# Optimization experiments

Hardware: AMD Instinct MI355X
Metric: run time of the kernel (lower is better)

The kernel has to match this reference:

```python
import jax, jax.numpy as jnp
import numpy as np
from jax import lax

N, T, D_IN = 8192, 64, 64
R = 256            # reservoir_dim
K = 3              # diffusion hops
D_OUT = 64
E = 131072
LEAK = 0.3
SPECTRAL_RADIUS = 0.9
SPARSITY = 0.9


def setup_inputs() -> dict:
    key = jax.random.key(0)
    kx, ke = jax.random.split(key)
    rng = np.random.default_rng(0)

    # ESN fixed buffers (match torch init: randn*0.1; sparse randn scaled to rho)
    W_in = (rng.standard_normal((R, D_IN)) * 0.1).astype(np.float32)
    W_res = rng.standard_normal((R, R)).astype(np.float32)
    mask = rng.random((R, R)) < SPARSITY
    W_res[mask] = 0.0
    rho = float(np.abs(np.linalg.eigvals(W_res)).max())
    if rho > 1e-8:
        W_res = W_res * (SPECTRAL_RADIUS / rho)

    # readout: Linear((K+1)*R -> 2*D_OUT), GELU, Linear(2*D_OUT -> D_OUT), LayerNorm
    fan1 = (K + 1) * R
    W1 = (rng.standard_normal((2 * D_OUT, fan1)) / np.sqrt(fan1)).astype(np.float32)
    b1 = np.zeros((2 * D_OUT,), np.float32)
    W2 = (rng.standard_normal((D_OUT, 2 * D_OUT)) / np.sqrt(2 * D_OUT)).astype(np.float32)
    b2 = np.zeros((D_OUT,), np.float32)
    gamma = np.ones((D_OUT,), np.float32)
    beta = np.zeros((D_OUT,), np.float32)

    x = jax.random.normal(kx, (N, T, D_IN), dtype=jnp.float32)
    edge_index = jax.random.randint(ke, (2, E), 0, N, dtype=jnp.int64)

    return {
        "x": x,
        "edge_index": edge_index,
        "W_in": jnp.asarray(W_in),
        "W_res": jnp.asarray(W_res),
        "W1": jnp.asarray(W1), "b1": jnp.asarray(b1),
        "W2": jnp.asarray(W2), "b2": jnp.asarray(b2),
        "gamma": jnp.asarray(gamma), "beta": jnp.asarray(beta),
    }


def _esn(x, W_in, W_res):
    # x: [N, T, D_IN] -> final reservoir state [N, R]
    x_proj = jnp.einsum("ntd,rd->tnr", x, W_in)  # [T, N, R]

    def step(h, xp_t):
        h_new = jnp.tanh(xp_t + h @ W_res.T)
        return (1.0 - LEAK) * h + LEAK * h_new, None

    h0 = jnp.zeros((x.shape[0], W_res.shape[0]), dtype=x.dtype)
    h, _ = lax.scan(step, h0, x_proj)
    return h


def _norm_adj(edge_index, n_nodes):
    # symmetric D^{-1/2} A D^{-1/2}; dedup handled by idempotent .set
    row = jnp.concatenate([edge_index[0], edge_index[1]])
    col = jnp.concatenate([edge_index[1], edge_index[0]])
    A_bin = jnp.zeros((n_nodes, n_nodes), jnp.float32).at[row, col].set(1.0)
    deg = A_bin.sum(axis=1)
    dinv = jnp.where(deg > 0, 1.0 / jnp.sqrt(jnp.maximum(deg, 1e-12)), 0.0)
    dinv = jnp.minimum(dinv, 1e6)
    return dinv[:, None] * A_bin * dinv[None, :]


def reference(x, edge_index, W_in, W_res, W1, b1, W2, b2, gamma, beta):
    h = _esn(x, W_in, W_res)                    # [N, R]
    A = _norm_adj(edge_index, x.shape[0])       # [N, N]

    diffused = [h]
    h_k = h
    for _ in range(K):
        h_k = A @ h_k
        diffused.append(h_k)
    cat = jnp.concatenate(diffused, axis=-1)    # [N, (K+1)*R]

    z = jax.nn.gelu(cat @ W1.T + b1, approximate=False)
    z = z @ W2.T + b2                           # [N, D_OUT]
    mu = z.mean(axis=-1, keepdims=True)
    var = z.var(axis=-1, keepdims=True)
    z = (z - mu) / jnp.sqrt(var + 1e-5)
    return z * gamma + beta
```

## Files before the change

kernel.cpp:

```cpp
#include <hip/hip_runtime.h>
#include <hip/hip_bf16.h>
#include <hip/hip_fp16.h>
#include <math.h>

#define NN    8192
#define TT    64
#define DIN   64
#define RR    256
#define DOUT  64
#define HID   128
#define CATD  1024
#define NE    131072
#define MASKW 256
#define MAXD  256
#define HROW  328

typedef __attribute__((ext_vector_type(8))) short    s16x8;
typedef __attribute__((ext_vector_type(8))) _Float16 f16x8;
typedef __attribute__((ext_vector_type(4))) float    f32x4;

static __device__ __forceinline__ unsigned short f2bs(float f) {
  union { __hip_bfloat16 b; unsigned short u; } cv;
  cv.b = __float2bfloat16(f);
  return cv.u;
}
static __device__ __forceinline__ unsigned int pack2bf(float a, float b) {
  return (unsigned int)f2bs(a) | ((unsigned int)f2bs(b) << 16);
}
static __device__ __forceinline__ unsigned int pack2h(float a, float b) {
  return (unsigned int)__half_as_ushort(__float2half(a))
       | ((unsigned int)__half_as_ushort(__float2half(b)) << 16);
}


__global__ __launch_bounds__(256) void zero_mask_kernel(uint4* mask4, int n4) {
  int i = blockIdx.x * 256 + threadIdx.x;
  if (i < n4) mask4[i] = make_uint4(0u, 0u, 0u, 0u);
}

__global__ __launch_bounds__(256) void edge_kernel(const int* __restrict__ eidx,
                                                   unsigned int* __restrict__ mask) {
  int e = blockIdx.x * 256 + threadIdx.x;
  if (e < NE) {
    int u = eidx[e];
    int v = eidx[NE + e];
    atomicOr(&mask[(size_t)u * MASKW + (v >> 5)], 1u << (v & 31));
    atomicOr(&mask[(size_t)v * MASKW + (u >> 5)], 1u << (u & 31));
  }
}

__global__ __launch_bounds__(256) void nbrlist_kernel(const unsigned int* __restrict__ mask,
                                                      unsigned short* __restrict__ nbrlist,
                                                      int* __restrict__ nbrcnt,
                                                      float* __restrict__ dinv) {
  __shared__ int wsum[4];
  const int n = blockIdx.x;
  const int tid = threadIdx.x;
  const int lane = tid & 63;
  const int w = tid >> 6;
  unsigned int m = mask[(size_t)n * MASKW + tid];
  const int c = __popc(m);
  int inc = c;
#pragma unroll
  for (int d = 1; d < 64; d <<= 1) {
    int v = __shfl_up(inc, d, 64);
    if (lane >= d) inc += v;
  }
  if (lane == 63) wsum[w] = inc;
  __syncthreads();
  int base = 0;
  for (int i = 0; i < w; ++i) base += wsum[i];
  int off = base + inc - c;
  while (m) {
    int b = __ffs(m) - 1;
    m &= m - 1;
    if (off < MAXD) nbrlist[(size_t)n * MAXD + off] = (unsigned short)(tid * 32 + b);
    ++off;
  }
  if (tid == 255) {
    int tot = base + inc;
    nbrcnt[n] = tot < MAXD ? tot : MAXD;
    dinv[n] = (tot > 0) ? fminf(rsqrtf((float)tot), 1e6f) : 0.0f;
  }
}

__global__ __launch_bounds__(256) void cvt_weights_kernel(
    const float* __restrict__ Wres, const float* __restrict__ Win,
    const float* __restrict__ W1, const float* __restrict__ W2,
    unsigned short* __restrict__ wresh, unsigned short* __restrict__ winh,
    unsigned short* __restrict__ W1h, unsigned short* __restrict__ W2h) {
  int i = blockIdx.x * 256 + threadIdx.x;
  if (i < 65536) wresh[i] = f2bs(Wres[i]);
  else if (i < 81920) winh[i - 65536] = f2bs(Win[i - 65536]);
  else if (i < 212992) W1h[i - 81920] = __half_as_ushort(__float2half(W1[i - 81920]));
  else if (i < 221184) W2h[i - 212992] = __half_as_ushort(__float2half(W2[i - 212992]));
}

__global__ __launch_bounds__(512, 4) void esn_mfma_kernel(
    const float* __restrict__ x,
    const unsigned short* __restrict__ winh,
    const unsigned short* __restrict__ wresh,
    unsigned short* __restrict__ cat)
{
  __shared__ unsigned short hs[2][16][HROW];
  const int tid  = threadIdx.x;
  const int lane = tid & 63;
  const int w    = tid >> 6;
  const int lr   = lane & 15;
  const int lg   = lane >> 4;
  const int sn   = tid >> 5;
  const int sq   = tid & 31;
  const long gn0 = (long)blockIdx.x * 16;
  const int bx   = (lr >> 3) & 1;
  const int lgx  = lg ^ bx;
  const int lgw  = (lg >> 1) ^ bx;
  const int bs   = (sn >> 3) & 1;

  s16x8 waug[2][10];
#pragma unroll
  for (int rt = 0; rt < 2; ++rt) {
    const int r = w * 32 + rt * 16 + lr;
#pragma unroll
    for (int kt = 0; kt < 8; ++kt)
      waug[rt][kt] = *(const s16x8*)(wresh + r * RR + kt * 32 + lg * 8);
#pragma unroll
    for (int kt = 8; kt < 10; ++kt)
      waug[rt][kt] = *(const s16x8*)(winh + r * DIN + (kt - 8) * 32 + lg * 8);
  }

  unsigned short* const rd0 = &hs[0][0][0] + lr * HROW + lgx * 8;
  unsigned short* const rd1 = &hs[1][0][0] + lr * HROW + lgx * 8;
  unsigned short* const wh0 = &hs[0][0][0] + lr * HROW + (w * 4 + lgw) * 8 + (lg & 1) * 4;
  unsigned short* const wh1 = &hs[1][0][0] + lr * HROW + (w * 4 + lgw) * 8 + (lg & 1) * 4;
  unsigned short* const xs0 = &hs[0][0][0] + sn * HROW + (32 + ((sq >> 2) ^ bs)) * 8 + (sq & 3) * 2;
  unsigned short* const xs1 = &hs[1][0][0] + sn * HROW + (32 + ((sq >> 2) ^ bs)) * 8 + (sq & 3) * 2;

  for (int i = tid; i < 16 * HROW / 2; i += 512) ((unsigned int*)hs[0])[i] = 0u;

  const float* xrow = x + (gn0 + sn) * (long)(TT * DIN) + sq * 2;
  float2 xr0 = *(const float2*)(xrow);
  float2 xr1 = *(const float2*)(xrow + DIN);
  __syncthreads();
  *(unsigned int*)xs0 = pack2bf(xr0.x, xr0.y);
  xr0 = *(const float2*)(xrow + 2 * DIN);

  f32x4 hreg[2];
  hreg[0] = (f32x4){0.f, 0.f, 0.f, 0.f};
  hreg[1] = (f32x4){0.f, 0.f, 0.f, 0.f};
  __syncthreads();

#define ESN_STEP(RD, WH, XS, XRS, XRL, TNEXT)                                        \
  {                                                                                  \
    f32x4 a0e = (f32x4){0.f,0.f,0.f,0.f}, a0o = a0e, a1e = a0e, a1o = a0e;           \
    __builtin_amdgcn_s_setprio(1);                                                   \
    _Pragma("unroll")                                                                \
    for (int kt = 0; kt < 10; kt += 2) {                                             \
      const s16x8 hbe = *(const s16x8*)(RD + kt * 32);                               \
      const s16x8 hbo = *(const s16x8*)(RD + (kt + 1) * 32);                         \
      a0e = __builtin_amdgcn_mfma_f32_16x16x32_bf16(waug[0][kt], hbe, a0e, 0, 0, 0); \
      a1e = __builtin_amdgcn_mfma_f32_16x16x32_bf16(waug[1][kt], hbe, a1e, 0, 0, 0); \
      a0o = __builtin_amdgcn_mfma_f32_16x16x32_bf16(waug[0][kt+1], hbo, a0o, 0, 0, 0);\
      a1o = __builtin_amdgcn_mfma_f32_16x16x32_bf16(waug[1][kt+1], hbo, a1o, 0, 0, 0);\
    }                                                                                \
    __builtin_amdgcn_s_setprio(0);                                                   \
    *(unsigned int*)(XS) = pack2bf(XRS.x, XRS.y);                 \
    XRL = *(const float2*)(xrow + (TNEXT) * DIN);                      \
    _Pragma("unroll")                                                                \
    for (int rt = 0; rt < 2; ++rt) {                                                 \
      const f32x4 ae = rt ? a1e : a0e;                                               \
      const f32x4 ao = rt ? a1o : a0o;                                               \
      f32x4 hn;                                                                      \
      _Pragma("unroll")                                                              \
      for (int i = 0; i < 4; ++i) {                                                  \
        const float sacc = ae[i] + ao[i];                                            \
        const float e = __builtin_amdgcn_exp2f(sacc * 2.8853900817779268f);          \
        const float rc = __builtin_amdgcn_rcpf(e + 1.0f);                            \
        hn[i] = fmaf(-0.6f, rc, fmaf(0.7f, hreg[rt][i], 0.3f));                      \
      }                                                                              \
      hreg[rt] = hn;                                                                 \
      *(uint2*)(WH + rt * 16) =                                                      \
          make_uint2(pack2bf(hn[0], hn[1]), pack2bf(hn[2], hn[3]));                  \
    }                                                                                \
  }

  for (int tc = 0; tc < TT / 2; ++tc) {
    const int t = tc * 2;
    const int tla = (t + 3 < TT) ? t + 3 : TT - 1;
    ESN_STEP(rd0, wh1, xs1, xr1, xr1, tla);
    __syncthreads();
    const int tlb = (t + 4 < TT) ? t + 4 : TT - 1;
    ESN_STEP(rd1, wh0, xs0, xr0, xr0, tlb);
    __syncthreads();
  }
#undef ESN_STEP

#pragma unroll
  for (int rt = 0; rt < 2; ++rt) {
    *(uint2*)(cat + (gn0 + lr) * CATD + w * 32 + rt * 16 + lg * 4) =
        make_uint2(pack2h(hreg[rt][0], hreg[rt][1]), pack2h(hreg[rt][2], hreg[rt][3]));
  }
}

__global__ __launch_bounds__(256) void spmv_kernel(
    const unsigned short* __restrict__ nbrlist, const int* __restrict__ nbrcnt,
    const float* __restrict__ dinv, unsigned short* __restrict__ cat, int hop)
{
  const int wv   = threadIdx.x >> 6;
  const int lane = threadIdx.x & 63;
  const int half = lane >> 5;
  const int li   = lane & 31;
  const int n    = blockIdx.x * 8 + wv * 2 + half;
  const int cnt  = nbrcnt[n];
  const __half* in = (const __half*)cat + (size_t)(hop - 1) * RR;
  float acc[8];
#pragma unroll
  for (int k = 0; k < 8; ++k) acc[k] = 0.0f;

  for (int c0 = 0; c0 < cnt; c0 += 32) {
    const int m = (cnt - c0 < 32) ? cnt - c0 : 32;
    int idx = 0; float dv = 0.f;
    if (li < m) {
      idx = (int)nbrlist[(size_t)n * MAXD + c0 + li];
      dv  = dinv[idx];
    }
#pragma unroll 8
    for (int i = 0; i < m; ++i) {
      const int   j  = __shfl(idx, half * 32 + i, 64);
      const float wj = __shfl(dv,  half * 32 + i, 64);
      const uint4 u  = *(const uint4*)(in + (size_t)j * CATD + li * 8);
      const float2 f0 = __half22float2(*(const __half2*)&u.x);
      const float2 f1 = __half22float2(*(const __half2*)&u.y);
      const float2 f2 = __half22float2(*(const __half2*)&u.z);
      const float2 f3 = __half22float2(*(const __half2*)&u.w);
      acc[0] += wj * f0.x; acc[1] += wj * f0.y;
      acc[2] += wj * f1.x; acc[3] += wj * f1.y;
      acc[4] += wj * f2.x; acc[5] += wj * f2.y;
      acc[6] += wj * f3.x; acc[7] += wj * f3.y;
    }
  }
  const float dn = dinv[n];
  uint4 o;
  o.x = pack2h(acc[0] * dn, acc[1] * dn);
  o.y = pack2h(acc[2] * dn, acc[3] * dn);
  o.z = pack2h(acc[4] * dn, acc[5] * dn);
  o.w = pack2h(acc[6] * dn, acc[7] * dn);
  *(uint4*)(cat + (size_t)n * CATD + (size_t)hop * RR + li * 8) = o;
}

__global__ __launch_bounds__(256) void readout_kernel(
    const unsigned short* __restrict__ cat,
    const unsigned short* __restrict__ W1h,
    const float* __restrict__ b1,
    const unsigned short* __restrict__ W2h,
    const float* __restrict__ b2, const float* __restrict__ gamma,
    const float* __restrict__ beta, float* __restrict__ out)
{
  __shared__ unsigned short z1[32][136];
  __shared__ float z2[32][68];
  const int tid  = threadIdx.x;
  const int lane = tid & 63;
  const int w    = tid >> 6;
  const int lr   = lane & 15;
  const int lg   = lane >> 4;
  const long gn0 = (long)blockIdx.x * 32;

  f32x4 a00 = (f32x4){0.f,0.f,0.f,0.f}, a01 = a00, a10 = a00, a11 = a00;
  const unsigned short* arow0 = cat + (gn0 + lr) * CATD;
  const unsigned short* arow1 = cat + (gn0 + 16 + lr) * CATD;
  const unsigned short* brow0 = W1h + (w * 32 + lr) * CATD;
  const unsigned short* brow1 = W1h + (w * 32 + 16 + lr) * CATD;
#pragma unroll 8
  for (int kt = 0; kt < 32; ++kt) {
    const f16x8 af0 = *(const f16x8*)(arow0 + kt * 32 + lg * 8);
    const f16x8 af1 = *(const f16x8*)(arow1 + kt * 32 + lg * 8);
    const f16x8 bf0 = *(const f16x8*)(brow0 + kt * 32 + lg * 8);
    const f16x8 bf1 = *(const f16x8*)(brow1 + kt * 32 + lg * 8);
    a00 = __builtin_amdgcn_mfma_f32_16x16x32_f16(af0, bf0, a00, 0, 0, 0);
    a01 = __builtin_amdgcn_mfma_f32_16x16x32_f16(af0, bf1, a01, 0, 0, 0);
    a10 = __builtin_amdgcn_mfma_f32_16x16x32_f16(af1, bf0, a10, 0, 0, 0);
    a11 = __builtin_amdgcn_mfma_f32_16x16x32_f16(af1, bf1, a11, 0, 0, 0);
  }
  const float is2 = 0.70710678118654752f;
#pragma unroll
  for (int nt = 0; nt < 2; ++nt) {
#pragma unroll
    for (int ht = 0; ht < 2; ++ht) {
      const int hid = w * 32 + ht * 16 + lr;
      const float bb = b1[hid];
      const f32x4 a = nt ? (ht ? a11 : a10) : (ht ? a01 : a00);
#pragma unroll
      for (int i = 0; i < 4; ++i) {
        const float v = a[i] + bb;
        const float g = 0.5f * v * (1.0f + erff(v * is2));
        z1[nt * 16 + lg * 4 + i][hid] = __half_as_ushort(__float2half(g));
      }
    }
  }
  __syncthreads();

  f32x4 c20 = (f32x4){0.f,0.f,0.f,0.f}, c21 = c20;
  const unsigned short* w2row = W2h + (w * 16 + lr) * HID;
#pragma unroll
  for (int kt = 0; kt < 4; ++kt) {
    const f16x8 bf  = *(const f16x8*)(w2row + kt * 32 + lg * 8);
    const f16x8 af0 = *(const f16x8*)(&z1[lr][kt * 32 + lg * 8]);
    const f16x8 af1 = *(const f16x8*)(&z1[16 + lr][kt * 32 + lg * 8]);
    c20 = __builtin_amdgcn_mfma_f32_16x16x32_f16(af0, bf, c20, 0, 0, 0);
    c21 = __builtin_amdgcn_mfma_f32_16x16x32_f16(af1, bf, c21, 0, 0, 0);
  }
  {
    const float bb = b2[w * 16 + lr];
#pragma unroll
    for (int i = 0; i < 4; ++i) {
      z2[lg * 4 + i][w * 16 + lr]      = c20[i] + bb;
      z2[16 + lg * 4 + i][w * 16 + lr] = c21[i] + bb;
    }
  }
  __syncthreads();

  {
    const int n = tid >> 3;
    const int c = tid & 7;
    float v[8], s = 0.0f, s2 = 0.0f;
#pragma unroll
    for (int k2 = 0; k2 < 8; ++k2) {
      v[k2] = z2[n][c + 8 * k2];
      s += v[k2]; s2 += v[k2] * v[k2];
    }
#pragma unroll
    for (int m = 1; m < 8; m <<= 1) {
      s  += __shfl_xor(s,  m, 64);
      s2 += __shfl_xor(s2, m, 64);
    }
    const float mu  = s * (1.0f / 64.0f);
    const float var = s2 * (1.0f / 64.0f) - mu * mu;
    const float inv = rsqrtf(var + 1e-5f);
    float* orow = out + (gn0 + n) * DOUT;
#pragma unroll
    for (int k2 = 0; k2 < 8; ++k2)
      orow[c + 8 * k2] = (v[k2] - mu) * inv * gamma[c + 8 * k2] + beta[c + 8 * k2];
  }
}


extern "C" void kernel_launch(void* const* d_in, const int* in_sizes, int n_in,
                              void* d_out, int out_size, void* d_ws, size_t ws_size,
                              hipStream_t stream) {
  const float* x     = (const float*)d_in[0];
  const int*   eidx  = (const int*)d_in[1];
  const float* W_in  = (const float*)d_in[2];
  const float* W_res = (const float*)d_in[3];
  const float* W1    = (const float*)d_in[4];
  const float* b1    = (const float*)d_in[5];
  const float* W2    = (const float*)d_in[6];
  const float* b2    = (const float*)d_in[7];
  const float* gamma = (const float*)d_in[8];
  const float* beta  = (const float*)d_in[9];
  float* out = (float*)d_out;

  char* ws = (char*)d_ws;
  size_t off = 0;
  auto alloc = [&](size_t bytes) {
    void* p = ws + off;
    off += (bytes + 255) & ~(size_t)255;
    return p;
  };
  unsigned int*   mask    = (unsigned int*)  alloc((size_t)NN * MASKW * 4);
  unsigned short* cat     = (unsigned short*)alloc((size_t)NN * CATD * 2);
  unsigned short* nbrlist = (unsigned short*)alloc((size_t)NN * MAXD * 2);
  int*            nbrcnt  = (int*)           alloc((size_t)NN * 4);
  float*          dinv    = (float*)         alloc((size_t)NN * 4);
  unsigned short* wresh   = (unsigned short*)alloc((size_t)RR * RR * 2);
  unsigned short* winh    = (unsigned short*)alloc((size_t)RR * DIN * 2);
  unsigned short* W1h     = (unsigned short*)alloc((size_t)HID * CATD * 2);
  unsigned short* W2h     = (unsigned short*)alloc((size_t)DOUT * HID * 2);

  zero_mask_kernel<<<2048, 256, 0, stream>>>((uint4*)mask, NN * MASKW / 4);
  edge_kernel<<<NE / 256, 256, 0, stream>>>(eidx, mask);
  nbrlist_kernel<<<NN, 256, 0, stream>>>(mask, nbrlist, nbrcnt, dinv);
  cvt_weights_kernel<<<864, 256, 0, stream>>>(W_res, W_in, W1, W2, wresh, winh, W1h, W2h);

  esn_mfma_kernel<<<NN / 16, 512, 0, stream>>>(x, winh, wresh, cat);

  for (int k = 1; k <= 3; ++k)
    spmv_kernel<<<NN / 8, 256, 0, stream>>>(nbrlist, nbrcnt, dinv, cat, k);

  readout_kernel<<<NN / 32, 256, 0, stream>>>(cat, W1h, b1, W2h, b2, gamma, beta, out);
}
```

Before: 193.0 us.

## Gather SpMV neighbor features from an FP8 shadow copy and fuse setup kernels

```diff
diff --git a/kernel.cpp b/kernel.cpp
--- a/kernel.cpp
+++ b/kernel.cpp
@@ -14,10 +14,12 @@
 #define MASKW 256
 #define MAXD  256
 #define HROW  328
+#define C8ROW 768
 
 typedef __attribute__((ext_vector_type(8))) short    s16x8;
 typedef __attribute__((ext_vector_type(8))) _Float16 f16x8;
 typedef __attribute__((ext_vector_type(4))) float    f32x4;
+typedef __attribute__((ext_vector_type(2))) float    f32x2;
 
 static __device__ __forceinline__ unsigned short f2bs(float f) {
   union { __hip_bfloat16 b; unsigned short u; } cv;
@@ -31,11 +33,26 @@
   return (unsigned int)__half_as_ushort(__float2half(a))
        | ((unsigned int)__half_as_ushort(__float2half(b)) << 16);
 }
-
-
-__global__ __launch_bounds__(256) void zero_mask_kernel(uint4* mask4, int n4) {
+static __device__ __forceinline__ unsigned int pack4fp8(float a, float b, float c, float d) {
+  unsigned int p = 0;
+  p = __builtin_amdgcn_cvt_pk_fp8_f32(a, b, (int)p, false);
+  p = __builtin_amdgcn_cvt_pk_fp8_f32(c, d, (int)p, true);
+  return p;
+}
+
+
+__global__ __launch_bounds__(256) void setup_kernel(
+    uint4* __restrict__ mask4,
+    const float* __restrict__ Wres, const float* __restrict__ Win,
+    const float* __restrict__ W1, const float* __restrict__ W2,
+    unsigned short* __restrict__ wresh, unsigned short* __restrict__ winh,
+    unsigned short* __restrict__ W1h, unsigned short* __restrict__ W2h) {
   int i = blockIdx.x * 256 + threadIdx.x;
-  if (i < n4) mask4[i] = make_uint4(0u, 0u, 0u, 0u);
+  mask4[i] = make_uint4(0u, 0u, 0u, 0u);
+  if (i < 65536) wresh[i] = f2bs(Wres[i]);
+  else if (i < 81920) winh[i - 65536] = f2bs(Win[i - 65536]);
+  else if (i < 212992) W1h[i - 81920] = __half_as_ushort(__float2half(W1[i - 81920]));
+  else if (i < 221184) W2h[i - 212992] = __half_as_ushort(__float2half(W2[i - 212992]));
 }
 
 __global__ __launch_bounds__(256) void edge_kernel(const int* __restrict__ eidx,
@@ -84,23 +101,12 @@
   }
 }
 
-__global__ __launch_bounds__(256) void cvt_weights_kernel(
-    const float* __restrict__ Wres, const float* __restrict__ Win,
-    const float* __restrict__ W1, const float* __restrict__ W2,
-    unsigned short* __restrict__ wresh, unsigned short* __restrict__ winh,
-    unsigned short* __restrict__ W1h, unsigned short* __restrict__ W2h) {
-  int i = blockIdx.x * 256 + threadIdx.x;
-  if (i < 65536) wresh[i] = f2bs(Wres[i]);
-  else if (i < 81920) winh[i - 65536] = f2bs(Win[i - 65536]);
-  else if (i < 212992) W1h[i - 81920] = __half_as_ushort(__float2half(W1[i - 81920]));
-  else if (i < 221184) W2h[i - 212992] = __half_as_ushort(__float2half(W2[i - 212992]));
-}
-
 __global__ __launch_bounds__(512, 4) void esn_mfma_kernel(
     const float* __restrict__ x,
     const unsigned short* __restrict__ winh,
     const unsigned short* __restrict__ wresh,
-    unsigned short* __restrict__ cat)
+    unsigned short* __restrict__ cat,
+    unsigned char* __restrict__ cat8)
 {
   __shared__ unsigned short hs[2][16][HROW];
   const int tid  = threadIdx.x;
@@ -198,12 +204,15 @@
   for (int rt = 0; rt < 2; ++rt) {
     *(uint2*)(cat + (gn0 + lr) * CATD + w * 32 + rt * 16 + lg * 4) =
         make_uint2(pack2h(hreg[rt][0], hreg[rt][1]), pack2h(hreg[rt][2], hreg[rt][3]));
+    *(unsigned int*)(cat8 + (gn0 + lr) * C8ROW + w * 32 + rt * 16 + lg * 4) =
+        pack4fp8(hreg[rt][0], hreg[rt][1], hreg[rt][2], hreg[rt][3]);
   }
 }
 
 __global__ __launch_bounds__(256) void spmv_kernel(
     const unsigned short* __restrict__ nbrlist, const int* __restrict__ nbrcnt,
-    const float* __restrict__ dinv, unsigned short* __restrict__ cat, int hop)
+    const float* __restrict__ dinv, unsigned short* __restrict__ cat,
+    unsigned char* __restrict__ cat8, int hop)
 {
   const int wv   = threadIdx.x >> 6;
   const int lane = threadIdx.x & 63;
@@ -211,7 +220,7 @@
   const int li   = lane & 31;
   const int n    = blockIdx.x * 8 + wv * 2 + half;
   const int cnt  = nbrcnt[n];
-  const __half* in = (const __half*)cat + (size_t)(hop - 1) * RR;
+  const unsigned char* in8 = cat8 + (size_t)(hop - 1) * RR;
   float acc[8];
 #pragma unroll
   for (int k = 0; k < 8; ++k) acc[k] = 0.0f;
@@ -227,24 +236,32 @@
     for (int i = 0; i < m; ++i) {
       const int   j  = __shfl(idx, half * 32 + i, 64);
       const float wj = __shfl(dv,  half * 32 + i, 64);
-      const uint4 u  = *(const uint4*)(in + (size_t)j * CATD + li * 8);
-      const float2 f0 = __half22float2(*(const __half2*)&u.x);
-      const float2 f1 = __half22float2(*(const __half2*)&u.y);
-      const float2 f2 = __half22float2(*(const __half2*)&u.z);
-      const float2 f3 = __half22float2(*(const __half2*)&u.w);
-      acc[0] += wj * f0.x; acc[1] += wj * f0.y;
-      acc[2] += wj * f1.x; acc[3] += wj * f1.y;
-      acc[4] += wj * f2.x; acc[5] += wj * f2.y;
-      acc[6] += wj * f3.x; acc[7] += wj * f3.y;
+      const uint2 u  = *(const uint2*)(in8 + (size_t)j * C8ROW + li * 8);
+      const f32x2 f0 = __builtin_amdgcn_cvt_pk_f32_fp8((int)u.x, false);
+      const f32x2 f1 = __builtin_amdgcn_cvt_pk_f32_fp8((int)u.x, true);
+      const f32x2 f2 = __builtin_amdgcn_cvt_pk_f32_fp8((int)u.y, false);
+      const f32x2 f3 = __builtin_amdgcn_cvt_pk_f32_fp8((int)u.y, true);
+      acc[0] += wj * f0[0]; acc[1] += wj * f0[1];
+      acc[2] += wj * f1[0]; acc[3] += wj * f1[1];
+      acc[4] += wj * f2[0]; acc[5] += wj * f2[1];
+      acc[6] += wj * f3[0]; acc[7] += wj * f3[1];
     }
   }
   const float dn = dinv[n];
+#pragma unroll
+  for (int k = 0; k < 8; ++k) acc[k] *= dn;
   uint4 o;
-  o.x = pack2h(acc[0] * dn, acc[1] * dn);
-  o.y = pack2h(acc[2] * dn, acc[3] * dn);
-  o.z = pack2h(acc[4] * dn, acc[5] * dn);
-  o.w = pack2h(acc[6] * dn, acc[7] * dn);
+  o.x = pack2h(acc[0], acc[1]);
+  o.y = pack2h(acc[2], acc[3]);
+  o.z = pack2h(acc[4], acc[5]);
+  o.w = pack2h(acc[6], acc[7]);
   *(uint4*)(cat + (size_t)n * CATD + (size_t)hop * RR + li * 8) = o;
+  if (hop < 3) {
+    uint2 o8;
+    o8.x = pack4fp8(acc[0], acc[1], acc[2], acc[3]);
+    o8.y = pack4fp8(acc[4], acc[5], acc[6], acc[7]);
+    *(uint2*)(cat8 + (size_t)n * C8ROW + (size_t)hop * RR + li * 8) = o8;
+  }
 }
 
 __global__ __launch_bounds__(256) void readout_kernel(
@@ -367,6 +384,7 @@
   };
   unsigned int*   mask    = (unsigned int*)  alloc((size_t)NN * MASKW * 4);
   unsigned short* cat     = (unsigned short*)alloc((size_t)NN * CATD * 2);
+  unsigned char*  cat8    = (unsigned char*) alloc((size_t)NN * C8ROW);
   unsigned short* nbrlist = (unsigned short*)alloc((size_t)NN * MAXD * 2);
   int*            nbrcnt  = (int*)           alloc((size_t)NN * 4);
   float*          dinv    = (float*)         alloc((size_t)NN * 4);
@@ -375,15 +393,15 @@
   unsigned short* W1h     = (unsigned short*)alloc((size_t)HID * CATD * 2);
   unsigned short* W2h     = (unsigned short*)alloc((size_t)DOUT * HID * 2);
 
-  zero_mask_kernel<<<2048, 256, 0, stream>>>((uint4*)mask, NN * MASKW / 4);
+  setup_kernel<<<2048, 256, 0, stream>>>((uint4*)mask, W_res, W_in, W1, W2,
+                                         wresh, winh, W1h, W2h);
   edge_kernel<<<NE / 256, 256, 0, stream>>>(eidx, mask);
   nbrlist_kernel<<<NN, 256, 0, stream>>>(mask, nbrlist, nbrcnt, dinv);
-  cvt_weights_kernel<<<864, 256, 0, stream>>>(W_res, W_in, W1, W2, wresh, winh, W1h, W2h);
-
-  esn_mfma_kernel<<<NN / 16, 512, 0, stream>>>(x, winh, wresh, cat);
+
+  esn_mfma_kernel<<<NN / 16, 512, 0, stream>>>(x, winh, wresh, cat, cat8);
 
   for (int k = 1; k <= 3; ++k)
-    spmv_kernel<<<NN / 8, 256, 0, stream>>>(nbrlist, nbrcnt, dinv, cat, k);
+    spmv_kernel<<<NN / 8, 256, 0, stream>>>(nbrlist, nbrcnt, dinv, cat, cat8, k);
 
   readout_kernel<<<NN / 32, 256, 0, stream>>>(cat, W1h, b1, W2h, b2, gamma, beta, out);
 }
```

After: 188.0 us. -2.6%, faster.
